# Optimization experiments

Measured on AMD Instinct MI355X. Metric: run time of the kernel, lower is better.

The kernel has to match this reference:

```python
import jax, jax.numpy as jnp
import numpy as np

MS = 0.001
TAU = 50.0
THRESHOLD = 1.0


def setup_inputs() -> dict:
    key = jax.random.key(0)
    kx, kw = jax.random.split(key)
    x = jax.random.normal(kx, (32, 1024, 1000), dtype=jnp.float32)
    # nn.init.normal_(w, mean=0.0, std=8000)
    w = jax.random.normal(kw, (1024, 1024), dtype=jnp.float32) * 8000.0
    return {"x": x, "w": w}


def reference(x, w):
    # x: [B, n_in, T], w: [n_in, n_out]
    # Precompute all input currents in one batched GEMM: [T, B, n_out]
    currents = jnp.einsum('bit,io->tbo', x, w)

    def step(v, cur):
        v = v + (-v + cur) * (MS / TAU)
        spikes = (v >= THRESHOLD).astype(v.dtype)
        v = v * (1.0 - spikes)
        return v, spikes

    v0 = jnp.zeros((x.shape[0], w.shape[1]), dtype=x.dtype)
    _, out = jax.lax.scan(step, v0, currents)  # out: [T, B, n_out]
    return jnp.transpose(out, (1, 2, 0))  # [B, n_out, T]
```

## Files before the change

### kernel.cpp

```cpp
#include <hip/hip_runtime.h>


#define NB 32
#define NI 1024
#define NO 1024
#define NT 1000
#define NS 6
#define BT 64
#define BO 64
#define KI 32
#define NKB (NI/KI)
#define TILEB (NS*2*64*16)

typedef int i32x4  __attribute__((ext_vector_type(4)));
typedef int i32x16 __attribute__((ext_vector_type(16)));

typedef const __attribute__((address_space(1))) void GVOID;
typedef __attribute__((address_space(3))) void LVOID;
#define GLDS16(g, l) __builtin_amdgcn_global_load_lds((GVOID*)(g), (LVOID*)(l), 16, 0, 0)

__global__ void snn_wscale(const float* __restrict__ w, float* __restrict__ sb)
{
    __shared__ float red[4][64];
    const int tid = threadIdx.x;
    const int ol = tid & 63, iq = tid >> 6;
    const int o = blockIdx.x * 64 + ol;
    float m = 0.f;
    for (int i = iq; i < NI; i += 4) m = fmaxf(m, fabsf(w[(size_t)i * NO + o]));
    red[iq][ol] = m;
    __syncthreads();
    if (iq == 0) {
        m = fmaxf(fmaxf(red[0][ol], red[1][ol]), fmaxf(red[2][ol], red[3][ol]));
        const int e = (__float_as_uint(m) >> 23) & 255;
        float S = 0.f, Si = 0.f;
        if (e) {
            S  = __uint_as_float((unsigned)(e + 1) << 23);
            Si = __uint_as_float((unsigned)(253 - e) << 23);
        }
        sb[o] = S;
        sb[NO + o] = Si;
    }
}

__global__ void snn_wslice(const float* __restrict__ w, const float* __restrict__ sb,
                           signed char* __restrict__ wp)
{
    __shared__ int sldw[NS][64][16];
    const int tid = threadIdx.x;
    const int ol = tid & 63, iq = tid >> 6;
    const int o0 = blockIdx.x * 64, ic = blockIdx.y * 64;
    const float inv = sb[NO + o0 + ol];
#pragma unroll
    for (int q4 = 0; q4 < 16; q4 += 4) {
        int pk[NS] = {0, 0, 0, 0, 0, 0};
#pragma unroll
        for (int j = 0; j < 4; ++j) {
            const int i = ic + iq * 16 + q4 + j;
            float wv = w[(size_t)i * NO + o0 + ol] * inv;
#pragma unroll
            for (int s = 0; s < NS; ++s) {
                const float f = wv * 128.f;
                const int a = (int)f;
                wv = f - (float)a;
                pk[s] |= (a & 255) << (8 * j);
            }
        }
        const int cdw = (iq * 16 + q4) >> 2;
#pragma unroll
        for (int s = 0; s < NS; ++s) sldw[s][ol][cdw ^ (ol & 15)] = pk[s];
    }
    __syncthreads();
    signed char* tb = wp + (size_t)blockIdx.x * (NKB * TILEB) + (size_t)(ic >> 5) * TILEB;
#pragma unroll
    for (int p = 0; p < 24; ++p) {
        const int idx = p * 256 + tid;
        const int kbi = idx >= 3072;
        const int ld  = idx - (kbi ? 3072 : 0);
        const int s  = ld >> 9;
        const int kc = (ld >> 8) & 1;
        const int r  = (ld >> 2) & 63;
        const int d4 = ld & 3;
        *(int*)&tb[(size_t)kbi * TILEB + (size_t)ld * 4] =
            sldw[s][r][(kbi * 8 + kc * 4 + d4) ^ (r & 15)];
    }
}

__global__ void snn_xscale(const float* __restrict__ x, float* __restrict__ sa,
                           int t0, int tca)
{
    __shared__ float red[4][64];
    const int tid = threadIdx.x;
    const int tl = tid & 63, iq = tid >> 6;
    const int b = blockIdx.y;
    const int tt = blockIdx.x * 64;
    const int tg = t0 + tt + tl;
    const float* xb = x + (size_t)b * NI * NT;
    float m = 0.f;
    if (tg < NT)
        for (int i = iq; i < NI; i += 4) m = fmaxf(m, fabsf(xb[(size_t)i * NT + tg]));
    red[iq][tl] = m;
    __syncthreads();
    if (iq == 0) {
        m = fmaxf(fmaxf(red[0][tl], red[1][tl]), fmaxf(red[2][tl], red[3][tl]));
        const int e = (__float_as_uint(m) >> 23) & 255;
        sa[(size_t)b * tca + tt + tl] = e ? __uint_as_float((unsigned)(e + 1) << 23) : 0.f;
    }
}

__global__ void snn_xslice(const float* __restrict__ x, const float* __restrict__ sa,
                           signed char* __restrict__ xp, int t0, int tca, int ntiles)
{
    __shared__ int sldw[NS][64][16];
    const int tid = threadIdx.x;
    const int tl = tid & 63, iq = tid >> 6;
    const int b = blockIdx.y;
    const int tile = blockIdx.x;
    const int tg = t0 + tile * 64 + tl;
    const bool valid = (tg < NT);
    const float* xb = x + (size_t)b * NI * NT;
    const float S = sa[(size_t)b * tca + tile * 64 + tl];
    const float inv = (S > 0.f)
        ? __uint_as_float((254u - (__float_as_uint(S) >> 23)) << 23) : 0.f;
    signed char* tb = xp + (size_t)(b * ntiles + tile) * (NKB * TILEB);

    for (int c4 = 0; c4 < 4; ++c4) {
        const int ic = blockIdx.z * 256 + c4 * 64;
#pragma unroll
        for (int q4 = 0; q4 < 16; q4 += 4) {
            int pk[NS] = {0, 0, 0, 0, 0, 0};
#pragma unroll
            for (int j = 0; j < 4; ++j) {
                const int i = ic + iq * 16 + q4 + j;
                float wv = valid ? xb[(size_t)i * NT + tg] * inv : 0.f;
#pragma unroll
                for (int s = 0; s < NS; ++s) {
                    const float f = wv * 128.f;
                    const int a = (int)f;
                    wv = f - (float)a;
                    pk[s] |= (a & 255) << (8 * j);
                }
            }
            const int cdw = (iq * 16 + q4) >> 2;
#pragma unroll
            for (int s = 0; s < NS; ++s) sldw[s][tl][cdw ^ (tl & 15)] = pk[s];
        }
        __syncthreads();
        signed char* kbb = tb + (size_t)(ic >> 5) * TILEB;
#pragma unroll
        for (int p = 0; p < 24; ++p) {
            const int idx = p * 256 + tid;
            const int kbi = idx >= 3072;
            const int ld  = idx - (kbi ? 3072 : 0);
            const int s  = ld >> 9;
            const int kc = (ld >> 8) & 1;
            const int r  = (ld >> 2) & 63;
            const int d4 = ld & 3;
            *(int*)&kbb[(size_t)kbi * TILEB + (size_t)ld * 4] =
                sldw[s][r][(kbi * 8 + kc * 4 + d4) ^ (r & 15)];
        }
        __syncthreads();
    }
}

__global__ __launch_bounds__(256, 2)
void snn_gemm_i8(const signed char* __restrict__ xp, const signed char* __restrict__ wp,
                 const float* __restrict__ sa, const float* __restrict__ sb,
                 double* __restrict__ cur, int t0, int tca, int ntiles)
{
    __shared__ signed char As[3][TILEB];
    __shared__ signed char Bs[3][TILEB];

    const int tid  = threadIdx.x;
    const int lane = tid & 63;
    const int wave = tid >> 6;
    const int wm = (wave >> 1) * 32;
    const int wn = (wave & 1) * 32;
    const int l31 = lane & 31;
    const int hi  = lane >> 5;

    int lid = blockIdx.x + (int)gridDim.x * (blockIdx.y + (int)gridDim.y * blockIdx.z);
    {
        const int nwg = (int)(gridDim.x * gridDim.y * gridDim.z);
        const int q = nwg >> 3, r = nwg & 7;
        const int xcd = lid & 7, off = lid >> 3;
        lid = (xcd < r ? xcd * (q + 1) : r * (q + 1) + (xcd - r) * q) + off;
    }
    const int ox  = lid & 15;
    const int rst = lid >> 4;
    const int ty  = rst % ntiles;
    const int b   = rst / ntiles;

    const int o0 = ox * BO;
    const int bt = ty * BT;

    int prow[16];
    {
        i32x4 pa, pb;
#pragma unroll
        for (int q = 0; q < 4; ++q) {
            int va = 0, vb = 0;
#pragma unroll
            for (int jj = 0; jj < 4; ++jj) {
                const int k = 16 * hi + q * 4 + jj;
                if (l31 == k) va |= 1 << (8 * jj);
                vb |= (k & 255) << (8 * jj);
            }
            pa[q] = va; pb[q] = vb;
        }
        i32x16 pp = (i32x16)0;
        pp = __builtin_amdgcn_mfma_i32_32x32x32_i8(pa, pb, pp, 0, 0, 0);
#pragma unroll
        for (int r = 0; r < 16; ++r) prow[r] = pp[r] & 31;
    }

    i32x16 acc[NS];
#pragma unroll
    for (int c = 0; c < NS; ++c) acc[c] = (i32x16)0;

    const signed char* Ag = xp + (size_t)(b * ntiles + ty) * (NKB * TILEB) + tid * 16;
    const signed char* Bg = wp + (size_t)ox * (NKB * TILEB) + tid * 16;
    signed char* Al = &As[0][0] + wave * 1024;
    signed char* Bl = &Bs[0][0] + wave * 1024;

#define STAGE(src, bsel) do {                                                  \
    _Pragma("unroll")                                                          \
    for (int u = 0; u < 3; ++u) {                                              \
        GLDS16(Ag + (size_t)(src) * TILEB + u * 4096,                          \
               Al + (bsel) * TILEB + u * 4096);                                \
        GLDS16(Bg + (size_t)(src) * TILEB + u * 4096,                          \
               Bl + (bsel) * TILEB + u * 4096);                                \
    } } while (0)

    STAGE(0, 0);
    STAGE(1, 1);

    const int abase = hi * 1024 + (wm + l31) * 16;
    const int bbase = hi * 1024 + (wn + l31) * 16;

    for (int kb = 0; kb < NKB; ++kb) {
        int src = kb + 2; if (src >= NKB) src -= NKB;
        STAGE(src, (kb + 2) % 3);
        asm volatile("s_waitcnt vmcnt(12)" ::: "memory");
        __builtin_amdgcn_s_barrier();

        const signed char* Ab = &As[kb % 3][0];
        const signed char* Bb = &Bs[kb % 3][0];
        i32x4 af[NS], bf[NS];
#pragma unroll
        for (int s = 0; s < NS; ++s) {
            af[s] = *(const i32x4*)&Ab[abase + s * 2048];
            bf[s] = *(const i32x4*)&Bb[bbase + s * 2048];
        }
#pragma unroll
        for (int i = 0; i < NS; ++i)
#pragma unroll
            for (int c = NS - 1; c >= i; --c)
                acc[c] = __builtin_amdgcn_mfma_i32_32x32x32_i8(
                    af[i], bf[c - i], acc[c], 0, 0, 0);

        asm volatile("s_waitcnt lgkmcnt(0)" ::: "memory");
        __builtin_amdgcn_sched_barrier(0);
        __builtin_amdgcn_s_barrier();
    }
#undef STAGE

    const double c128[NS] = {0x1p-14, 0x1p-21, 0x1p-28, 0x1p-35, 0x1p-42, 0x1p-49};
    const int ocol = o0 + wn + l31;
    const double sbv = (double)sb[ocol];
#pragma unroll
    for (int r = 0; r < 16; ++r) {
        const int trow = bt + wm + prow[r];
        double v = 0.0;
#pragma unroll
        for (int c = 0; c < NS; ++c) v += (double)acc[c][r] * c128[c];
        v *= (double)sa[(size_t)b * tca + trow] * sbv;
        if (t0 + trow < NT)
            cur[((size_t)trow * NB + b) * NO + ocol] = v;
    }
}

#define NC 32
__global__ __launch_bounds__(64)
void snn_scan_f64(const double* __restrict__ cur, float* __restrict__ out,
                  double* __restrict__ vstate, int t0, int len)
{
    const int gid = blockIdx.x * 64 + threadIdx.x;
    const double dt = 0.001 / 50.0;

    double v = (t0 == 0) ? 0.0 : vstate[gid];
    const double* cp = cur + gid;
    float* op = out + (size_t)gid * NT + t0;

    const size_t ts = (size_t)NB * NO;
    const int nb = len / NC;
    const int rem = len - nb * NC;

    double A[NC], B[NC];
#pragma unroll
    for (int j = 0; j < NC; ++j) A[j] = (j < len) ? cp[(size_t)j * ts] : 0.0;

    for (int blk = 0; blk < nb; ++blk) {
        const int next = (blk + 1) * NC;
#pragma unroll
        for (int j = 0; j < NC; ++j)
            B[j] = (next + j < len) ? cp[(size_t)(next + j) * ts] : 0.0;

#pragma unroll
        for (int q = 0; q < NC; q += 8) {
            float s[8];
#pragma unroll
            for (int j = 0; j < 8; ++j) {
                v = v + (A[q + j] - v) * dt;
                const bool sp = (v >= 1.0);
                s[j] = sp ? 1.0f : 0.0f;
                if (sp) v = 0.0;
            }
            *(float4*)(op + q)     = make_float4(s[0], s[1], s[2], s[3]);
            *(float4*)(op + q + 4) = make_float4(s[4], s[5], s[6], s[7]);
        }
        op += NC;
#pragma unroll
        for (int j = 0; j < NC; ++j) A[j] = B[j];
    }

    for (int q = 0; q < rem; q += 8) {
        float s[8];
#pragma unroll
        for (int j = 0; j < 8; ++j) {
            v = v + (A[q + j] - v) * dt;
            const bool sp = (v >= 1.0);
            s[j] = sp ? 1.0f : 0.0f;
            if (sp) v = 0.0;
        }
        *(float4*)(op + q)     = make_float4(s[0], s[1], s[2], s[3]);
        *(float4*)(op + q + 4) = make_float4(s[4], s[5], s[6], s[7]);
    }
    vstate[gid] = v;
}

extern "C" void kernel_launch(void* const* d_in, const int* in_sizes, int n_in,
                              void* d_out, int out_size, void* d_ws, size_t ws_size,
                              hipStream_t stream)
{
    const float* x = (const float*)d_in[0];
    const float* w = (const float*)d_in[1];
    float* out = (float*)d_out;

    char* p = (char*)d_ws;
    double* vstate = (double*)p;         p += (size_t)NB * NO * 8;
    float* sbv = (float*)p;              p += (size_t)2 * NO * 4;
    signed char* wp = (signed char*)p;   p += (size_t)(NO / 64) * NKB * TILEB;

    const size_t fixed = (size_t)(p - (char*)d_ws);
    const size_t per_t = (size_t)NB * 4
                       + (size_t)NS * NB * NI
                       + (size_t)NB * NO * 8;
    int tca = 512;
    while (tca > 64 && fixed + (size_t)tca * per_t > ws_size) tca -= 64;

    float* sa = (float*)p;               p += (size_t)NB * tca * 4;
    signed char* xpl = (signed char*)p;  p += (size_t)NB * (tca / 64) * NKB * TILEB;
    double* cur = (double*)p;

    snn_wscale<<<dim3(NO / 64), dim3(256), 0, stream>>>(w, sbv);
    snn_wslice<<<dim3(NO / 64, NI / 64), dim3(256), 0, stream>>>(w, sbv, wp);

    for (int t0 = 0; t0 < NT; t0 += tca) {
        const int len = (NT - t0 < tca) ? (NT - t0) : tca;
        const int ntiles = (len + BT - 1) / BT;
        snn_xscale<<<dim3(ntiles, NB), dim3(256), 0, stream>>>(x, sa, t0, tca);
        snn_xslice<<<dim3(ntiles, NB, 4), dim3(256), 0, stream>>>(x, sa, xpl, t0, tca, ntiles);
        snn_gemm_i8<<<dim3(NO / BO, ntiles, NB), dim3(256), 0, stream>>>(
            xpl, wp, sa, sbv, cur, t0, tca, ntiles);
        snn_scan_f64<<<dim3((NB * NO) / 64), dim3(64), 0, stream>>>(
            cur, out, vstate, t0, len);
    }
}
```

Measured before the change: 1.289 ms.

## Double-buffer LDS fragments in registers to overlap ds_reads with MFMAs

Restructures the int8 MFMA GEMM main loop so the LDS fragments for the next k-block load into a second register set while MFMAs consume the current set. The loop is unrolled by two with ping-pong fragment buffers, rotating slot counters replace the modulo arithmetic, and one combined wait plus barrier is used per stage instead of two barriers. MFMA sections run under raised s_setprio. The aim is to hide LDS read latency behind matrix ops, at the cost of twice the fragment registers and a possible hit to occupancy.

Measured after the change: 1.289 ms. About the same (-0.0%).

```diff
diff --git a/kernel.cpp b/kernel.cpp
--- a/kernel.cpp
+++ b/kernel.cpp
@@ -231,38 +231,67 @@
                Bl + (bsel) * TILEB + u * 4096);                                \
     } } while (0)
 
+    const int abase = hi * 1024 + (wm + l31) * 16;
+    const int bbase = hi * 1024 + (wn + l31) * 16;
+
+#define LDFRAG(fa, fb, slot) do {                                              \
+    const signed char* Ab_ = &As[slot][0];                                     \
+    const signed char* Bb_ = &Bs[slot][0];                                     \
+    _Pragma("unroll")                                                          \
+    for (int s = 0; s < NS; ++s) {                                             \
+        fa[s] = *(const i32x4*)&Ab_[abase + s * 2048];                         \
+        fb[s] = *(const i32x4*)&Bb_[bbase + s * 2048];                         \
+    } } while (0)
+
+#define MFMAS(fa, fb) do {                                                     \
+    __builtin_amdgcn_s_setprio(1);                                             \
+    _Pragma("unroll")                                                          \
+    for (int i = 0; i < NS; ++i)                                               \
+    _Pragma("unroll")                                                          \
+    for (int c = NS - 1; c >= i; --c)                                          \
+        acc[c] = __builtin_amdgcn_mfma_i32_32x32x32_i8(fa[i], fb[c - i],       \
+                                                       acc[c], 0, 0, 0);       \
+    __builtin_amdgcn_s_setprio(0);                                             \
+    } while (0)
+
+#define SYNC() do {                                                            \
+    asm volatile("s_waitcnt vmcnt(6)" ::: "memory");                           \
+    asm volatile("s_waitcnt lgkmcnt(0)" ::: "memory");                         \
+    __builtin_amdgcn_sched_barrier(0);                                         \
+    __builtin_amdgcn_s_barrier();                                              \
+    } while (0)
+
+    i32x4 fa0[NS], fb0[NS], fa1[NS], fb1[NS];
+
     STAGE(0, 0);
     STAGE(1, 1);
-
-    const int abase = hi * 1024 + (wm + l31) * 16;
-    const int bbase = hi * 1024 + (wn + l31) * 16;
-
-    for (int kb = 0; kb < NKB; ++kb) {
-        int src = kb + 2; if (src >= NKB) src -= NKB;
-        STAGE(src, (kb + 2) % 3);
-        asm volatile("s_waitcnt vmcnt(12)" ::: "memory");
-        __builtin_amdgcn_s_barrier();
-
-        const signed char* Ab = &As[kb % 3][0];
-        const signed char* Bb = &Bs[kb % 3][0];
-        i32x4 af[NS], bf[NS];
-#pragma unroll
-        for (int s = 0; s < NS; ++s) {
-            af[s] = *(const i32x4*)&Ab[abase + s * 2048];
-            bf[s] = *(const i32x4*)&Bb[bbase + s * 2048];
-        }
-#pragma unroll
-        for (int i = 0; i < NS; ++i)
-#pragma unroll
-            for (int c = NS - 1; c >= i; --c)
-                acc[c] = __builtin_amdgcn_mfma_i32_32x32x32_i8(
-                    af[i], bf[c - i], acc[c], 0, 0, 0);
-
-        asm volatile("s_waitcnt lgkmcnt(0)" ::: "memory");
-        __builtin_amdgcn_sched_barrier(0);
-        __builtin_amdgcn_s_barrier();
+    asm volatile("s_waitcnt vmcnt(6)" ::: "memory");
+    __builtin_amdgcn_s_barrier();
+    LDFRAG(fa0, fb0, 0);
+
+    int src = 2;
+    int st  = 2;
+    int rd  = 1;
+    for (int kb = 0; kb < NKB; kb += 2) {
+        STAGE(src, st);
+        src = (src + 1 >= NKB) ? 0 : src + 1;
+        st  = (st == 2) ? 0 : st + 1;
+        SYNC();
+        LDFRAG(fa1, fb1, rd);
+        rd  = (rd == 2) ? 0 : rd + 1;
+        MFMAS(fa0, fb0);
+        STAGE(src, st);
+        src = (src + 1 >= NKB) ? 0 : src + 1;
+        st  = (st == 2) ? 0 : st + 1;
+        SYNC();
+        LDFRAG(fa0, fb0, rd);
+        rd  = (rd == 2) ? 0 : rd + 1;
+        MFMAS(fa1, fb1);
     }
 #undef STAGE
+#undef LDFRAG
+#undef MFMAS
+#undef SYNC
 
     const double c128[NS] = {0x1p-14, 0x1p-21, 0x1p-28, 0x1p-35, 0x1p-42, 0x1p-49};
     const int ocol = o0 + wn + l31;
```

## Switch int8 GEMM to double-buffered LDS with 3 blocks per CU

Applied to the files above, without the earlier changes.

The GEMM pipeline goes from triple-buffered LDS staging with a prefetch distance of two to double buffering. This cuts LDS per block so launch bounds can ask for 3 blocks per CU. Inside each k-step, A fragments are loaded one ahead of the MFMAs and the MFMA groups run at raised wave priority. The permutation-row computation moves after the main loop to lower register pressure during it. The risk is that waiting on vmcnt(0) every iteration exposes global load latency that the deeper prefetch used to hide, and the tighter register budget may cause spills.

Result: faster. 1.209 ms (-6.2%).

```diff
diff --git a/kernel.cpp b/kernel.cpp
--- a/kernel.cpp
+++ b/kernel.cpp
@@ -162,13 +162,13 @@
     }
 }
 
-__global__ __launch_bounds__(256, 2)
+__global__ __launch_bounds__(256, 3)
 void snn_gemm_i8(const signed char* __restrict__ xp, const signed char* __restrict__ wp,
                  const float* __restrict__ sa, const float* __restrict__ sb,
                  double* __restrict__ cur, int t0, int tca, int ntiles)
 {
-    __shared__ signed char As[3][TILEB];
-    __shared__ signed char Bs[3][TILEB];
+    __shared__ signed char As[2][TILEB];
+    __shared__ signed char Bs[2][TILEB];
 
     const int tid  = threadIdx.x;
     const int lane = tid & 63;
@@ -192,26 +192,6 @@
 
     const int o0 = ox * BO;
     const int bt = ty * BT;
-
-    int prow[16];
-    {
-        i32x4 pa, pb;
-#pragma unroll
-        for (int q = 0; q < 4; ++q) {
-            int va = 0, vb = 0;
-#pragma unroll
-            for (int jj = 0; jj < 4; ++jj) {
-                const int k = 16 * hi + q * 4 + jj;
-                if (l31 == k) va |= 1 << (8 * jj);
-                vb |= (k & 255) << (8 * jj);
-            }
-            pa[q] = va; pb[q] = vb;
-        }
-        i32x16 pp = (i32x16)0;
-        pp = __builtin_amdgcn_mfma_i32_32x32x32_i8(pa, pb, pp, 0, 0, 0);
-#pragma unroll
-        for (int r = 0; r < 16; ++r) prow[r] = pp[r] & 31;
-    }
 
     i32x16 acc[NS];
 #pragma unroll
@@ -231,38 +211,64 @@
                Bl + (bsel) * TILEB + u * 4096);                                \
     } } while (0)
 
-    STAGE(0, 0);
-    STAGE(1, 1);
-
     const int abase = hi * 1024 + (wm + l31) * 16;
     const int bbase = hi * 1024 + (wn + l31) * 16;
 
-    for (int kb = 0; kb < NKB; ++kb) {
-        int src = kb + 2; if (src >= NKB) src -= NKB;
-        STAGE(src, (kb + 2) % 3);
-        asm volatile("s_waitcnt vmcnt(12)" ::: "memory");
-        __builtin_amdgcn_s_barrier();
-
-        const signed char* Ab = &As[kb % 3][0];
-        const signed char* Bb = &Bs[kb % 3][0];
-        i32x4 af[NS], bf[NS];
-#pragma unroll
-        for (int s = 0; s < NS; ++s) {
-            af[s] = *(const i32x4*)&Ab[abase + s * 2048];
-            bf[s] = *(const i32x4*)&Bb[bbase + s * 2048];
-        }
-#pragma unroll
-        for (int i = 0; i < NS; ++i)
-#pragma unroll
-            for (int c = NS - 1; c >= i; --c)
-                acc[c] = __builtin_amdgcn_mfma_i32_32x32x32_i8(
-                    af[i], bf[c - i], acc[c], 0, 0, 0);
-
+#define KITER(slot) do {                                                       \
+    const signed char* Ab_ = &As[slot][0];                                     \
+    const signed char* Bb_ = &Bs[slot][0];                                     \
+    i32x4 bf[NS];                                                              \
+    _Pragma("unroll")                                                          \
+    for (int s = 0; s < NS; ++s) bf[s] = *(const i32x4*)&Bb_[bbase + s * 2048];\
+    i32x4 a0 = *(const i32x4*)&Ab_[abase];                                     \
+    _Pragma("unroll")                                                          \
+    for (int i = 0; i < NS; ++i) {                                             \
+        i32x4 a1 = a0;                                                         \
+        if (i + 1 < NS) a1 = *(const i32x4*)&Ab_[abase + (i + 1) * 2048];      \
+        __builtin_amdgcn_s_setprio(1);                                         \
+        _Pragma("unroll")                                                      \
+        for (int c = NS - 1; c >= i; --c)                                      \
+            acc[c] = __builtin_amdgcn_mfma_i32_32x32x32_i8(a0, bf[c - i],      \
+                                                           acc[c], 0, 0, 0);   \
+        __builtin_amdgcn_s_setprio(0);                                         \
+        a0 = a1;                                                               \
+    } } while (0)
+
+    STAGE(0, 0);
+    asm volatile("s_waitcnt vmcnt(0)" ::: "memory");
+    __builtin_amdgcn_s_barrier();
+
+    for (int kb = 0; kb < NKB - 1; ++kb) {
+        STAGE(kb + 1, (kb + 1) & 1);
+        KITER(kb & 1);
+        asm volatile("s_waitcnt vmcnt(0)" ::: "memory");
         asm volatile("s_waitcnt lgkmcnt(0)" ::: "memory");
         __builtin_amdgcn_sched_barrier(0);
         __builtin_amdgcn_s_barrier();
     }
+    KITER((NKB - 1) & 1);
 #undef STAGE
+#undef KITER
+
+    int prow[16];
+    {
+        i32x4 pa, pb;
+#pragma unroll
+        for (int q = 0; q < 4; ++q) {
+            int va = 0, vb = 0;
+#pragma unroll
+            for (int jj = 0; jj < 4; ++jj) {
+                const int k = 16 * hi + q * 4 + jj;
+                if (l31 == k) va |= 1 << (8 * jj);
+                vb |= (k & 255) << (8 * jj);
+            }
+            pa[q] = va; pb[q] = vb;
+        }
+        i32x16 pp = (i32x16)0;
+        pp = __builtin_amdgcn_mfma_i32_32x32x32_i8(pa, pb, pp, 0, 0, 0);
+#pragma unroll
+        for (int r = 0; r < 16; ++r) prow[r] = pp[r] & 31;
+    }
 
     const double c128[NS] = {0x1p-14, 0x1p-21, 0x1p-28, 0x1p-35, 0x1p-42, 0x1p-49};
     const int ocol = o0 + wn + l31;
```
